# Kernel optimization log

Hardware: AMD Instinct MI355X
Metric: run time of the kernel (lower is better)

The kernel has to match this reference:

```python
import jax, jax.numpy as jnp
import numpy as np

N = 100_000   # nodes
E = 1_250_000 # edges
D = 64        # node feature dim
H = 64        # hidden_channels
C = 10        # num_classes
G = 128       # graphs in batch


def setup_inputs() -> dict:
    key = jax.random.key(0)
    ks = jax.random.split(key, 12)
    x = jax.random.normal(ks[0], (N, D), dtype=jnp.float32)
    edge_index = jax.random.randint(ks[1], (2, E), 0, N, dtype=jnp.int64)
    batch = jnp.sort(jax.random.randint(ks[2], (N,), 0, G, dtype=jnp.int64))
    s = lambda fan_in: 1.0 / np.sqrt(fan_in)
    W1 = jax.random.normal(ks[3], (D, H), dtype=jnp.float32) * s(D)
    b1 = jnp.zeros((H,), dtype=jnp.float32)
    W2 = jax.random.normal(ks[4], (H, H), dtype=jnp.float32) * s(H)
    b2 = jnp.zeros((H,), dtype=jnp.float32)
    W3 = jax.random.normal(ks[5], (H, H), dtype=jnp.float32) * s(H)
    b3 = jnp.zeros((H,), dtype=jnp.float32)
    Wl = jax.random.normal(ks[6], (H, C), dtype=jnp.float32) * s(H)
    bl = jnp.zeros((C,), dtype=jnp.float32)
    return {"x": x, "edge_index": edge_index, "batch": batch,
            "W1": W1, "b1": b1, "W2": W2, "b2": b2,
            "W3": W3, "b3": b3, "Wl": Wl, "bl": bl}


def _gcn_conv(h, W, b, src, dst, norm, n_nodes):
    # GCNConv: out[i] = sum_{e: dst(e)=i} norm_e * (h @ W)[src(e)] + b
    h = h @ W
    msg = h[src] * norm[:, None]                       # [E+N, H]
    return jax.ops.segment_sum(msg, dst, num_segments=n_nodes) + b


def reference(x, edge_index, batch, W1, b1, W2, b2, W3, b3, Wl, bl):
    x = x.astype(jnp.float32)
    ei = edge_index.astype(jnp.int64)
    # add self-loops (as PyG gcn_norm does by default)
    loop = jnp.arange(N, dtype=ei.dtype)
    src = jnp.concatenate([ei[0], loop])
    dst = jnp.concatenate([ei[1], loop])
    # symmetric normalization: deg over targets (in-degree incl. self-loops)
    deg = jax.ops.segment_sum(jnp.ones_like(src, dtype=jnp.float32), dst,
                              num_segments=N)
    dinv = jnp.where(deg > 0, jax.lax.rsqrt(jnp.maximum(deg, 1.0)), 0.0)
    norm = dinv[src] * dinv[dst]                       # [E+N]

    h = jax.nn.relu(_gcn_conv(x, W1, b1, src, dst, norm, N))
    h = jax.nn.relu(_gcn_conv(h, W2, b2, src, dst, norm, N))
    h = _gcn_conv(h, W3, b3, src, dst, norm, N)

    # global_mean_pool over graph ids
    ones = jnp.ones((N,), dtype=jnp.float32)
    counts = jax.ops.segment_sum(ones, batch, num_segments=G)
    sums = jax.ops.segment_sum(h, batch, num_segments=G)
    pooled = sums / jnp.maximum(counts, 1.0)[:, None]  # [G, H]

    # dropout is identity in eval mode
    return pooled @ Wl + bl                            # [G, C]
```

## Files before the change

### kernel.cpp

```cpp
#include <hip/hip_runtime.h>
#include <hip/hip_bf16.h>


#define BSHIFT 7
#define BNODES (1 << BSHIFT)
#define EPB    16384
#define MAXDEG 8192
#define MAXBUCKET 32768

typedef __attribute__((ext_vector_type(8))) short bf16x8;
typedef __attribute__((ext_vector_type(4))) float f32x4;

__device__ __forceinline__ void atomAddF(float* p, float v) {
#if defined(__gfx90a__) || defined(__gfx940__) || defined(__gfx941__) || defined(__gfx942__) || defined(__gfx950__)
    unsafeAtomicAdd(p, v);
#else
    atomicAdd(p, v);
#endif
}

__device__ __forceinline__ unsigned short f2bf(float x) {
    unsigned u = __float_as_uint(x);
    u += 0x7FFFu + ((u >> 16) & 1u);
    return (unsigned short)(u >> 16);
}
__device__ __forceinline__ float bf2f(unsigned short b) {
    return __uint_as_float((unsigned)b << 16);
}

__global__ __launch_bounds__(256)
void k_bhist(const int* __restrict__ dst, int* __restrict__ bcnt,
             int nE, int nBuckets) {
    __shared__ int cnt[1024];
    const int t = threadIdx.x;
    const int blk = blockIdx.x * EPB;
    for (int b = t; b < nBuckets; b += 256) cnt[b] = 0;
    __syncthreads();
#pragma unroll 4
    for (int i = 0; i < EPB / 256; i++) {
        int e = blk + i * 256 + t;
        if (e < nE) atomicAdd(&cnt[dst[e] >> BSHIFT], 1);
    }
    __syncthreads();
    for (int b = t; b < nBuckets; b += 256) {
        int c = cnt[b];
        if (c > 0) atomicAdd(&bcnt[b], c);
    }
}

__global__ void k_bscan(const int* __restrict__ bcnt, int* __restrict__ bbase,
                        int* __restrict__ bcur, int nb, int nE) {
    __shared__ int s[256];
    const int t = threadIdx.x;
    const int base = t * 4;
    int v0 = (base + 0 < nb) ? bcnt[base + 0] : 0;
    int v1 = (base + 1 < nb) ? bcnt[base + 1] : 0;
    int v2 = (base + 2 < nb) ? bcnt[base + 2] : 0;
    int v3 = (base + 3 < nb) ? bcnt[base + 3] : 0;
    int tsum = v0 + v1 + v2 + v3;
    s[t] = tsum;
    __syncthreads();
    for (int off = 1; off < 256; off <<= 1) {
        int val = 0;
        if (t >= off) val = s[t - off];
        __syncthreads();
        if (t >= off) s[t] += val;
        __syncthreads();
    }
    int excl = s[t] - tsum;
    if (base + 0 < nb) { bbase[base + 0] = excl;                bcur[base + 0] = excl; }
    if (base + 1 < nb) { bbase[base + 1] = excl + v0;           bcur[base + 1] = excl + v0; }
    if (base + 2 < nb) { bbase[base + 2] = excl + v0 + v1;      bcur[base + 2] = excl + v0 + v1; }
    if (base + 3 < nb) { bbase[base + 3] = excl + v0 + v1 + v2; bcur[base + 3] = excl + v0 + v1 + v2; }
    if (t == 0) bbase[nb] = nE;
}

__global__ __launch_bounds__(256)
void k_bucket(const int* __restrict__ src, const int* __restrict__ dst,
              int* __restrict__ bcur, int* __restrict__ staging,
              int nE, int nBuckets) {
    __shared__ int cnt[1024];
    __shared__ int lbase[1024];
    const int t = threadIdx.x;
    const int blk = blockIdx.x * EPB;

    for (int b = t; b < nBuckets; b += 256) cnt[b] = 0;
    __syncthreads();
#pragma unroll 4
    for (int i = 0; i < EPB / 256; i++) {
        int e = blk + i * 256 + t;
        if (e < nE) atomicAdd(&cnt[dst[e] >> BSHIFT], 1);
    }
    __syncthreads();
    for (int b = t; b < nBuckets; b += 256) {
        int c = cnt[b];
        if (c > 0) lbase[b] = atomicAdd(&bcur[b], c);
        cnt[b] = 0;
    }
    __syncthreads();
#pragma unroll 4
    for (int i = 0; i < EPB / 256; i++) {
        int e = blk + i * 256 + t;
        if (e < nE) {
            int s0 = src[e], d0 = dst[e];
            int b = d0 >> BSHIFT;
            int off = atomicAdd(&cnt[b], 1);
            int pos = lbase[b] + off;
            if ((unsigned)pos < (unsigned)nE)
                staging[pos] = (s0 << BSHIFT) | (d0 & (BNODES - 1));
        }
    }
}

__global__ __launch_bounds__(256)
void k_sort(const int* __restrict__ staging, const int* __restrict__ bbase,
            int* __restrict__ csr_s, int* __restrict__ rowptr,
            int* __restrict__ rowend, float* __restrict__ dinv,
            int n, int nE) {
    __shared__ int c[BNODES];
    __shared__ int sc[BNODES];
    __shared__ int cur[BNODES];
    const int t = threadIdx.x;
    const int b = blockIdx.x;
    const int node0 = b << BSHIFT;

    int seg0 = bbase[b];
    int seg1 = bbase[b + 1];
    seg0 = max(0, min(seg0, nE));
    seg1 = max(seg0, min(seg1, nE));
    seg1 = min(seg1, seg0 + MAXBUCKET);

    if (t < BNODES) c[t] = 0;
    __syncthreads();
    for (int e = seg0 + t; e < seg1; e += 256)
        atomicAdd(&c[staging[e] & (BNODES - 1)], 1);
    __syncthreads();
    if (t < BNODES) sc[t] = c[t];
    __syncthreads();
    for (int off = 1; off < BNODES; off <<= 1) {
        int v = 0;
        if (t >= off && t < BNODES) v = sc[t - off];
        __syncthreads();
        if (t >= off && t < BNODES) sc[t] += v;
        __syncthreads();
    }
    if (t < BNODES) {
        int excl = sc[t] - c[t];
        cur[t] = excl;
        int node = node0 + t;
        if (node < n) {
            rowptr[node] = seg0 + excl;
            rowend[node] = seg0 + excl + c[t];
            dinv[node]   = rsqrtf((float)c[t] + 1.0f);
        }
    }
    __syncthreads();
    for (int e = seg0 + t; e < seg1; e += 256) {
        int p = staging[e];
        int l = p & (BNODES - 1);
        int pos = seg0 + atomicAdd(&cur[l], 1);
        if ((unsigned)pos < (unsigned)nE)
            csr_s[pos] = ((unsigned)p) >> BSHIFT;
    }
}

__global__ __launch_bounds__(256)
void k_wfill(const int* __restrict__ csr_s, const float* __restrict__ dinv,
             float* __restrict__ csr_w, int nE, int n) {
    int e = blockIdx.x * blockDim.x + threadIdx.x;
    if (e < nE) {
        int s = csr_s[e];
        s = max(0, min(s, n - 1));
        csr_w[e] = dinv[s];
    }
}

__global__ void k_wprep(const float* __restrict__ W1, const float* __restrict__ W2,
                        const float* __restrict__ W3, unsigned short* __restrict__ Wt) {
    const float* W = (blockIdx.x == 0) ? W1 : ((blockIdx.x == 1) ? W2 : W3);
    unsigned short* o = Wt + blockIdx.x * 4096;
    for (int idx = threadIdx.x; idx < 4096; idx += 256) {
        int h = idx >> 6, k = idx & 63;
        o[idx] = f2bf(W[k * 64 + h]);
    }
}

template<bool RELU, typename AT>
__global__ __launch_bounds__(256)
void k_gemm(const AT* __restrict__ in, const unsigned short* __restrict__ Wt,
            const float* __restrict__ bias, unsigned short* __restrict__ out, int n) {
    const int lane = threadIdx.x & 63;
    const int wid  = threadIdx.x >> 6;
    const int col  = lane & 15;
    const int quad = lane >> 4;
    const int node0w = blockIdx.x * 64 + wid * 16;
    const int nodeA  = node0w + col;
    const bool validA = nodeA < n;

    f32x4 zero4 = {0.f, 0.f, 0.f, 0.f};
    f32x4 acc0 = zero4, acc1 = zero4, acc2 = zero4, acc3 = zero4;

#pragma unroll
    for (int ks = 0; ks < 64; ks += 32) {
        const int kb = ks + quad * 8;
        float a[8];
        if constexpr (sizeof(AT) == 4) {
            float4 a0 = make_float4(0.f, 0.f, 0.f, 0.f);
            float4 a1 = make_float4(0.f, 0.f, 0.f, 0.f);
            if (validA) {
                a0 = *(const float4*)((const float*)in + (size_t)nodeA * 64 + kb);
                a1 = *(const float4*)((const float*)in + (size_t)nodeA * 64 + kb + 4);
            }
            a[0] = a0.x; a[1] = a0.y; a[2] = a0.z; a[3] = a0.w;
            a[4] = a1.x; a[5] = a1.y; a[6] = a1.z; a[7] = a1.w;
        } else {
            ushort4 h0 = make_ushort4(0, 0, 0, 0), h1 = make_ushort4(0, 0, 0, 0);
            if (validA) {
                h0 = *(const ushort4*)((const unsigned short*)in + (size_t)nodeA * 64 + kb);
                h1 = *(const ushort4*)((const unsigned short*)in + (size_t)nodeA * 64 + kb + 4);
            }
            a[0] = bf2f(h0.x); a[1] = bf2f(h0.y); a[2] = bf2f(h0.z); a[3] = bf2f(h0.w);
            a[4] = bf2f(h1.x); a[5] = bf2f(h1.y); a[6] = bf2f(h1.z); a[7] = bf2f(h1.w);
        }
        if (RELU) {
#pragma unroll
            for (int i = 0; i < 8; i++) a[i] = fmaxf(a[i] + bias[kb + i], 0.f);
        }
        bf16x8 af;
#pragma unroll
        for (int i = 0; i < 8; i++) af[i] = (short)f2bf(a[i]);

        const bf16x8 b0f = *(const bf16x8*)(Wt + ((0 * 16 + col) * 64 + kb));
        const bf16x8 b1f = *(const bf16x8*)(Wt + ((1 * 16 + col) * 64 + kb));
        const bf16x8 b2f = *(const bf16x8*)(Wt + ((2 * 16 + col) * 64 + kb));
        const bf16x8 b3f = *(const bf16x8*)(Wt + ((3 * 16 + col) * 64 + kb));
        acc0 = __builtin_amdgcn_mfma_f32_16x16x32_bf16(af, b0f, acc0, 0, 0, 0);
        acc1 = __builtin_amdgcn_mfma_f32_16x16x32_bf16(af, b1f, acc1, 0, 0, 0);
        acc2 = __builtin_amdgcn_mfma_f32_16x16x32_bf16(af, b2f, acc2, 0, 0, 0);
        acc3 = __builtin_amdgcn_mfma_f32_16x16x32_bf16(af, b3f, acc3, 0, 0, 0);
    }

#pragma unroll
    for (int r = 0; r < 4; r++) {
        int nn = node0w + quad * 4 + r;
        if (nn < n) {
            size_t base = (size_t)nn * 64 + col;
            out[base +  0] = f2bf(acc0[r]);
            out[base + 16] = f2bf(acc1[r]);
            out[base + 32] = f2bf(acc2[r]);
            out[base + 48] = f2bf(acc3[r]);
        }
    }
}

template<int LAYER>
__global__ __launch_bounds__(256)
void k_agg(const unsigned short* __restrict__ hW, const int* __restrict__ rowptr,
           const int* __restrict__ rowend, const int* __restrict__ csr_s,
           const float* __restrict__ csr_w, const float* __restrict__ dinv,
           unsigned short* __restrict__ aggb, int n, int nE) {
    const int lane = threadIdx.x & 63;
    const int node = blockIdx.x * 4 + (threadIdx.x >> 6);
    if (node >= n) return;
    int row = rowptr[node];
    int end = rowend[node];
    row = max(0, min(row, nE));
    end = max(row, min(end, nE));
    end = min(end, row + MAXDEG);
    const float di = dinv[node];
    float acc0 = di * di * bf2f(hW[(size_t)node * 64 + lane]);
    float acc1 = 0.f, acc2 = 0.f, acc3 = 0.f;

    for (int base = row; base < end; base += 64) {
        const int m = min(64, end - base);
        int   s_l = 0;
        float w_l = 0.f;
        if (base + lane < end) {
            s_l = csr_s[base + lane];
            w_l = csr_w[base + lane] * di;
        }
        int j = 0;
        for (; j + 8 <= m; j += 8) {
            int   s0 = __shfl(s_l, j),     s1 = __shfl(s_l, j + 1);
            int   s2 = __shfl(s_l, j + 2), s3 = __shfl(s_l, j + 3);
            int   s4 = __shfl(s_l, j + 4), s5 = __shfl(s_l, j + 5);
            int   s6 = __shfl(s_l, j + 6), s7 = __shfl(s_l, j + 7);
            float w0 = __shfl(w_l, j),     w1 = __shfl(w_l, j + 1);
            float w2 = __shfl(w_l, j + 2), w3 = __shfl(w_l, j + 3);
            float w4 = __shfl(w_l, j + 4), w5 = __shfl(w_l, j + 5);
            float w6 = __shfl(w_l, j + 6), w7 = __shfl(w_l, j + 7);
            float h0 = bf2f(hW[(size_t)s0 * 64 + lane]);
            float h1 = bf2f(hW[(size_t)s1 * 64 + lane]);
            float h2 = bf2f(hW[(size_t)s2 * 64 + lane]);
            float h3 = bf2f(hW[(size_t)s3 * 64 + lane]);
            float h4 = bf2f(hW[(size_t)s4 * 64 + lane]);
            float h5 = bf2f(hW[(size_t)s5 * 64 + lane]);
            float h6 = bf2f(hW[(size_t)s6 * 64 + lane]);
            float h7 = bf2f(hW[(size_t)s7 * 64 + lane]);
            acc0 += w0 * h0 + w4 * h4;
            acc1 += w1 * h1 + w5 * h5;
            acc2 += w2 * h2 + w6 * h6;
            acc3 += w3 * h3 + w7 * h7;
        }
        for (; j + 2 <= m; j += 2) {
            int   s0 = __shfl(s_l, j),  s1 = __shfl(s_l, j + 1);
            float w0 = __shfl(w_l, j),  w1 = __shfl(w_l, j + 1);
            acc0 += w0 * bf2f(hW[(size_t)s0 * 64 + lane]);
            acc1 += w1 * bf2f(hW[(size_t)s1 * 64 + lane]);
        }
        for (; j < m; j++) {
            int   sj = __shfl(s_l, j);
            float wj = __shfl(w_l, j);
            acc0 += wj * bf2f(hW[(size_t)sj * 64 + lane]);
        }
    }
    aggb[(size_t)node * 64 + lane] = f2bf((acc0 + acc1) + (acc2 + acc3));
}


__global__ void k_pool(const unsigned short* __restrict__ aggb,
                       const int* __restrict__ batch,
                       float* __restrict__ pool, float* __restrict__ cnt, int n) {
    const int lane = threadIdx.x;
    const int base = blockIdx.x * 64;
    int g_cur = -1, run = 0;
    float acc = 0.f;
    for (int j = 0; j < 64; j++) {
        int node = base + j;
        if (node >= n) break;
        int g = batch[node];
        if (g != g_cur) {
            if (g_cur >= 0) {
                atomAddF(&pool[g_cur * 64 + lane], acc);
                if (lane == 0) atomAddF(&cnt[g_cur], (float)run);
            }
            g_cur = g; acc = 0.f; run = 0;
        }
        acc += bf2f(aggb[(size_t)node * 64 + lane]);
        run++;
    }
    if (g_cur >= 0) {
        atomAddF(&pool[g_cur * 64 + lane], acc);
        if (lane == 0) atomAddF(&cnt[g_cur], (float)run);
    }
}

__global__ void k_final(const float* __restrict__ pool, const float* __restrict__ cnt,
                        const float* __restrict__ b3, const float* __restrict__ Wl,
                        const float* __restrict__ bl, float* __restrict__ out) {
    __shared__ float s[64];
    const int g = blockIdx.x, t = threadIdx.x;
    float c = fmaxf(cnt[g], 1.0f);
    s[t] = pool[g * 64 + t] / c + b3[t];
    __syncthreads();
    if (t < 10) {
        float acc = bl[t];
#pragma unroll
        for (int k = 0; k < 64; k++) acc += s[k] * Wl[k * 10 + t];
        out[g * 10 + t] = acc;
    }
}

extern "C" void kernel_launch(void* const* d_in, const int* in_sizes, int n_in,
                              void* d_out, int out_size, void* d_ws, size_t ws_size,
                              hipStream_t stream) {
    const float* x   = (const float*)d_in[0];
    const int*   ei  = (const int*)d_in[1];
    const int*   bat = (const int*)d_in[2];
    const float* W1  = (const float*)d_in[3];
    const float* b1  = (const float*)d_in[4];
    const float* W2  = (const float*)d_in[5];
    const float* b2  = (const float*)d_in[6];
    const float* W3  = (const float*)d_in[7];
    const float* b3  = (const float*)d_in[8];
    const float* Wl  = (const float*)d_in[9];
    const float* bl  = (const float*)d_in[10];
    float* out = (float*)d_out;

    const int N_ = in_sizes[0] / 64;
    const int E_ = in_sizes[1] / 2;
    const int G_ = out_size / 10;
    const int NB_ = (N_ + BNODES - 1) >> BSHIFT;

    char* p = (char*)d_ws;
    int*   staging = (int*)p;   p += (size_t)E_ * 4;
    int*   csr_s  = (int*)p;    p += (size_t)E_ * 4;
    float* csr_w  = (float*)p;  p += (size_t)E_ * 4;
    unsigned short* aggb = (unsigned short*)p; p += (size_t)N_ * 64 * 2;
    unsigned short* hW   = (unsigned short*)p; p += (size_t)N_ * 64 * 2;
    float* dinv   = (float*)p;  p += (size_t)N_ * 4;
    int*   rowptr = (int*)p;    p += (size_t)N_ * 4;
    int*   rowend = (int*)p;    p += (size_t)N_ * 4;
    float* pool   = (float*)p;  p += (size_t)G_ * 64 * 4;
    float* cnt    = (float*)p;  p += (size_t)G_ * 4;
    unsigned short* Wt = (unsigned short*)p; p += 3 * 4096 * 2;
    int*   bcnt   = (int*)p;    p += (size_t)(NB_ + 1) * 4;
    int*   bbase  = (int*)p;    p += (size_t)(NB_ + 1) * 4;
    int*   bcur   = (int*)p;    p += (size_t)NB_ * 4;

    const int* srcp = ei;
    const int* dstp = ei + E_;

    hipMemsetAsync(bcnt, 0, (size_t)(NB_ + 1) * 4, stream);
    hipMemsetAsync(pool, 0, (size_t)(G_ * 64 + G_) * 4, stream);

    const int bin_blocks = (E_ + EPB - 1) / EPB;

    k_wprep<<<3, 256, 0, stream>>>(W1, W2, W3, Wt);
    k_bhist<<<bin_blocks, 256, 0, stream>>>(dstp, bcnt, E_, NB_);
    k_bscan<<<1, 256, 0, stream>>>(bcnt, bbase, bcur, NB_, E_);
    k_bucket<<<bin_blocks, 256, 0, stream>>>(srcp, dstp, bcur, staging, E_, NB_);
    k_sort<<<NB_, 256, 0, stream>>>(staging, bbase, csr_s, rowptr, rowend,
                                    dinv, N_, E_);
    k_wfill<<<(E_ + 255) / 256, 256, 0, stream>>>(csr_s, dinv, csr_w, E_, N_);

    const int gemm_blocks = (N_ + 63) / 64;
    const int agg_blocks  = (N_ + 3) / 4;

    k_gemm<false, float><<<gemm_blocks, 256, 0, stream>>>(x, Wt, nullptr, hW, N_);
    k_agg<1><<<agg_blocks, 256, 0, stream>>>(hW, rowptr, rowend, csr_s, csr_w,
                                             dinv, aggb, N_, E_);
    k_gemm<true, unsigned short><<<gemm_blocks, 256, 0, stream>>>(aggb, Wt + 4096,
                                                                  b1, hW, N_);
    k_agg<2><<<agg_blocks, 256, 0, stream>>>(hW, rowptr, rowend, csr_s, csr_w,
                                             dinv, aggb, N_, E_);
    k_gemm<true, unsigned short><<<gemm_blocks, 256, 0, stream>>>(aggb, Wt + 8192,
                                                                  b2, hW, N_);
    k_agg<3><<<agg_blocks, 256, 0, stream>>>(hW, rowptr, rowend, csr_s, csr_w,
                                             dinv, aggb, N_, E_);

    k_pool<<<(N_ + 63) / 64, 64, 0, stream>>>(aggb, bat, pool, cnt, N_);
    k_final<<<G_, 64, 0, stream>>>(pool, cnt, b3, Wl, bl, out);
}
```

Measured before the change: 392.1 us.

## Store per-block bucket histograms and column-scan them to drop the recount pass

The histogram kernel now writes per-block bucket counts to a global matrix instead of atomically merging them. A new column-scan kernel turns those counts into per-block exclusive offsets. The bucket kernel then reads its offsets directly and no longer recounts destinations or performs global atomics. It also halves the edges per block, giving more blocks. The cost is an extra serial column-scan kernel launch plus the workspace for the count matrix.

New measurement: 392.2 us. Within noise of the previous version (+0.0%).

```diff
diff --git a/kernel.cpp b/kernel.cpp
--- a/kernel.cpp
+++ b/kernel.cpp
@@ -4,7 +4,7 @@
 
 #define BSHIFT 7
 #define BNODES (1 << BSHIFT)
-#define EPB    16384
+#define EPB    8192
 #define MAXDEG 8192
 #define MAXBUCKET 32768
 
@@ -29,7 +29,7 @@
 }
 
 __global__ __launch_bounds__(256)
-void k_bhist(const int* __restrict__ dst, int* __restrict__ bcnt,
+void k_bhist(const int* __restrict__ dst, int* __restrict__ cnt_all,
              int nE, int nBuckets) {
     __shared__ int cnt[1024];
     const int t = threadIdx.x;
@@ -42,14 +42,27 @@
         if (e < nE) atomicAdd(&cnt[dst[e] >> BSHIFT], 1);
     }
     __syncthreads();
-    for (int b = t; b < nBuckets; b += 256) {
-        int c = cnt[b];
-        if (c > 0) atomicAdd(&bcnt[b], c);
-    }
+    for (int b = t; b < nBuckets; b += 256)
+        cnt_all[(size_t)blockIdx.x * nBuckets + b] = cnt[b];
+}
+
+__global__ __launch_bounds__(256)
+void k_colscan(int* __restrict__ cnt_all, int* __restrict__ bcnt,
+               int nBlocks, int nBuckets) {
+    int b = blockIdx.x * blockDim.x + threadIdx.x;
+    if (b >= nBuckets) return;
+    int running = 0;
+    for (int blk = 0; blk < nBlocks; blk++) {
+        size_t idx = (size_t)blk * nBuckets + b;
+        int v = cnt_all[idx];
+        cnt_all[idx] = running;
+        running += v;
+    }
+    bcnt[b] = running;
 }
 
 __global__ void k_bscan(const int* __restrict__ bcnt, int* __restrict__ bbase,
-                        int* __restrict__ bcur, int nb, int nE) {
+                        int nb, int nE) {
     __shared__ int s[256];
     const int t = threadIdx.x;
     const int base = t * 4;
@@ -68,33 +81,24 @@
         __syncthreads();
     }
     int excl = s[t] - tsum;
-    if (base + 0 < nb) { bbase[base + 0] = excl;                bcur[base + 0] = excl; }
-    if (base + 1 < nb) { bbase[base + 1] = excl + v0;           bcur[base + 1] = excl + v0; }
-    if (base + 2 < nb) { bbase[base + 2] = excl + v0 + v1;      bcur[base + 2] = excl + v0 + v1; }
-    if (base + 3 < nb) { bbase[base + 3] = excl + v0 + v1 + v2; bcur[base + 3] = excl + v0 + v1 + v2; }
+    if (base + 0 < nb) bbase[base + 0] = excl;
+    if (base + 1 < nb) bbase[base + 1] = excl + v0;
+    if (base + 2 < nb) bbase[base + 2] = excl + v0 + v1;
+    if (base + 3 < nb) bbase[base + 3] = excl + v0 + v1 + v2;
     if (t == 0) bbase[nb] = nE;
 }
 
 __global__ __launch_bounds__(256)
 void k_bucket(const int* __restrict__ src, const int* __restrict__ dst,
-              int* __restrict__ bcur, int* __restrict__ staging,
-              int nE, int nBuckets) {
+              const int* __restrict__ bbase, const int* __restrict__ cnt_all,
+              int* __restrict__ staging, int nE, int nBuckets) {
     __shared__ int cnt[1024];
     __shared__ int lbase[1024];
     const int t = threadIdx.x;
     const int blk = blockIdx.x * EPB;
 
-    for (int b = t; b < nBuckets; b += 256) cnt[b] = 0;
-    __syncthreads();
-#pragma unroll 4
-    for (int i = 0; i < EPB / 256; i++) {
-        int e = blk + i * 256 + t;
-        if (e < nE) atomicAdd(&cnt[dst[e] >> BSHIFT], 1);
-    }
-    __syncthreads();
     for (int b = t; b < nBuckets; b += 256) {
-        int c = cnt[b];
-        if (c > 0) lbase[b] = atomicAdd(&bcur[b], c);
+        lbase[b] = bbase[b] + cnt_all[(size_t)blockIdx.x * nBuckets + b];
         cnt[b] = 0;
     }
     __syncthreads();
@@ -381,6 +385,7 @@
     const int E_ = in_sizes[1] / 2;
     const int G_ = out_size / 10;
     const int NB_ = (N_ + BNODES - 1) >> BSHIFT;
+    const int bin_blocks = (E_ + EPB - 1) / EPB;
 
     char* p = (char*)d_ws;
     int*   staging = (int*)p;   p += (size_t)E_ * 4;
@@ -396,20 +401,19 @@
     unsigned short* Wt = (unsigned short*)p; p += 3 * 4096 * 2;
     int*   bcnt   = (int*)p;    p += (size_t)(NB_ + 1) * 4;
     int*   bbase  = (int*)p;    p += (size_t)(NB_ + 1) * 4;
-    int*   bcur   = (int*)p;    p += (size_t)NB_ * 4;
+    int*   cnt_all = (int*)p;   p += (size_t)bin_blocks * NB_ * 4;
 
     const int* srcp = ei;
     const int* dstp = ei + E_;
 
-    hipMemsetAsync(bcnt, 0, (size_t)(NB_ + 1) * 4, stream);
     hipMemsetAsync(pool, 0, (size_t)(G_ * 64 + G_) * 4, stream);
 
-    const int bin_blocks = (E_ + EPB - 1) / EPB;
-
     k_wprep<<<3, 256, 0, stream>>>(W1, W2, W3, Wt);
-    k_bhist<<<bin_blocks, 256, 0, stream>>>(dstp, bcnt, E_, NB_);
-    k_bscan<<<1, 256, 0, stream>>>(bcnt, bbase, bcur, NB_, E_);
-    k_bucket<<<bin_blocks, 256, 0, stream>>>(srcp, dstp, bcur, staging, E_, NB_);
+    k_bhist<<<bin_blocks, 256, 0, stream>>>(dstp, cnt_all, E_, NB_);
+    k_colscan<<<(NB_ + 255) / 256, 256, 0, stream>>>(cnt_all, bcnt, bin_blocks, NB_);
+    k_bscan<<<1, 256, 0, stream>>>(bcnt, bbase, NB_, E_);
+    k_bucket<<<bin_blocks, 256, 0, stream>>>(srcp, dstp, bbase, cnt_all,
+                                             staging, E_, NB_);
     k_sort<<<NB_, 256, 0, stream>>>(staging, bbase, csr_s, rowptr, rowend,
                                     dinv, N_, E_);
     k_wfill<<<(E_ + 255) / 256, 256, 0, stream>>>(csr_s, dinv, csr_w, E_, N_);
```
